# Kernel tuning notes

Hardware: AMD Instinct MI355X
Metric: run time of the kernel (lower is better)

Reference implementation:

```python
import jax, jax.numpy as jnp
import numpy as np

PATCH = 4      # patch_size
WIN = 8        # win_size (== win_stride, non-overlapping windows)
TAU = 0.05     # sinkhorn_tau
ITERS = 20     # sinkhorn_iters
EPS = 1e-6


def setup_inputs() -> dict:
    key = jax.random.key(0)
    k0, k1 = jax.random.split(key)
    B, C, H, W = 16, 4, 256, 256
    z0 = jax.random.normal(k0, (B, C, H, W), jnp.float32)
    z1 = jax.random.normal(k1, (B, C, H, W), jnp.float32)
    return {"z0": z0, "z1": z1}


def _token_feats(z):
    # patchify_latents + L2 normalize (F.normalize eps clamp). groupmean proj
    # is identity since d_match == token_dim.
    B, C, H, W = z.shape
    hp, wp = H // PATCH, W // PATCH
    t = z.reshape(B, C, hp, PATCH, wp, PATCH).transpose(0, 2, 4, 1, 3, 5)
    t = t.reshape(B, hp, wp, C * PATCH * PATCH)          # (B,hp,wp,D)
    n = jnp.maximum(jnp.sqrt(jnp.sum(t * t, axis=-1, keepdims=True)), EPS)
    return t / n


def _to_windows(f):
    B, hp, wp, D = f.shape
    nh, nw = hp // WIN, wp // WIN
    w = f.reshape(B, nh, WIN, nw, WIN, D).transpose(0, 1, 3, 2, 4, 5)
    return w.reshape(B * nh * nw, WIN * WIN, D)


def _sinkhorn_log(logits):
    # _sinkhorn_log_batch: alternate row (dim 2) / col (dim 1) logsumexp
    def step(lp, _):
        lp = lp - jax.nn.logsumexp(lp, axis=2, keepdims=True)
        lp = lp - jax.nn.logsumexp(lp, axis=1, keepdims=True)
        return lp, None
    lp, _ = jax.lax.scan(step, logits, None, length=ITERS)
    return lp


def _grid_sample_border(img, gx, gy):
    # F.grid_sample bilinear, padding_mode='border', align_corners=True,
    # with gx/gy already in absolute pixel coords (B,H,W).
    B, C, H, W = img.shape
    gx = jnp.clip(gx, 0.0, W - 1.0)
    gy = jnp.clip(gy, 0.0, H - 1.0)
    x0f = jnp.floor(gx); y0f = jnp.floor(gy)
    wx = (gx - x0f)[:, None]; wy = (gy - y0f)[:, None]   # (B,1,H,W)
    x0 = jnp.clip(x0f.astype(jnp.int32), 0, W - 1)
    x1 = jnp.clip(x0 + 1, 0, W - 1)
    y0 = jnp.clip(y0f.astype(jnp.int32), 0, H - 1)
    y1 = jnp.clip(y0 + 1, 0, H - 1)
    flat = img.reshape(B, C, H * W)

    def gat(yi, xi):
        idx = (yi * W + xi).reshape(B, 1, H * W)
        idx = jnp.broadcast_to(idx, (B, C, H * W))
        return jnp.take_along_axis(flat, idx, axis=2).reshape(B, C, H, W)

    v00 = gat(y0, x0); v01 = gat(y0, x1)
    v10 = gat(y1, x0); v11 = gat(y1, x1)
    return (v00 * (1 - wx) * (1 - wy) + v01 * wx * (1 - wy)
            + v10 * (1 - wx) * wy + v11 * wx * wy)


def reference(z0, z1):
    B, C, H, W = z0.shape
    hp, wp = H // PATCH, W // PATCH
    nh, nw = hp // WIN, wp // WIN
    f0 = _token_feats(z0)
    f1 = _token_feats(z1)
    w0 = _to_windows(f0)                                  # (BW, M, D)
    w1 = _to_windows(f1)
    logits = jnp.einsum('wid,wjd->wij', w0, w1) / TAU     # (BW, M, M)
    logp = _sinkhorn_log(logits)
    Pm = jax.nn.softmax(logp, axis=-1)                    # row-normalized plan
    # expected target position per source token (local window coords, x/y)
    ys, xs = jnp.meshgrid(jnp.arange(WIN), jnp.arange(WIN), indexing='ij')
    pos = jnp.stack([xs.ravel(), ys.ravel()], axis=-1).astype(z0.dtype)  # (M,2)
    disp = Pm @ pos - pos                                 # (BW, M, 2) token units
    disp = disp.reshape(B, nh, nw, WIN, WIN, 2).transpose(0, 1, 3, 2, 4, 5)
    disp = disp.reshape(B, hp, wp, 2)
    # token flow -> pixel flow (nearest upsample, scale by patch size)
    flow = jnp.repeat(jnp.repeat(disp, PATCH, axis=1), PATCH, axis=2) * PATCH
    yy, xx = jnp.meshgrid(jnp.arange(H, dtype=z0.dtype),
                          jnp.arange(W, dtype=z0.dtype), indexing='ij')
    gx = xx[None] + flow[..., 0]
    gy = yy[None] + flow[..., 1]
    return _grid_sample_border(z1, gx, gy)
```

## Files before the change

kernel.cpp:

```cpp
#include <hip/hip_runtime.h>
#include <math.h>


#define S0 68

__device__ __forceinline__ float rlane(float v, int l) {
    return __uint_as_float(__builtin_amdgcn_readlane(__float_as_uint(v), l));
}

__global__ __launch_bounds__(256, 1)
void skw_kernel(const float* __restrict__ z0, const float* __restrict__ z1,
                float* __restrict__ out) {
    __shared__ float f0 [64 * S0];
    __shared__ float f1t[64 * S0];
    __shared__ float Mw [4 * 64 * S0];
    __shared__ float psq0[256], psq1[256];
    __shared__ float invn0[64], invn1[64];
    __shared__ float dispxA[256], dispyA[256];

    const int t   = threadIdx.x;
    const int blk = blockIdx.x;
    const int b   = blk >> 4;
    const int wy  = (blk >> 1) & 7;
    const int wxq = blk & 1;
    const int Y0  = wy * 32;
    const int XB  = wxq * 128;

    const int xq = t & 7;
    const int yy = (t >> 3) & 31;
    const int mm = (yy >> 2) * 8 + xq;
    const int pi = yy & 3;

    const int wv   = t >> 6;
    const int lane = t & 63;

    #pragma unroll 1
    for (int w = 0; w < 4; ++w) {
        const int X0 = XB + w * 32;
        {
            const size_t base = (size_t)(b * 4) * 65536 + (size_t)(Y0 + yy) * 256 + X0 + xq * 4;
            const float* s0p = z0 + base;
            const float* s1p = z1 + base;
            float a0 = 0.f;
            #pragma unroll
            for (int c = 0; c < 4; ++c) {
                float4 vv = *(const float4*)(s0p + c * 65536);
                a0 += vv.x*vv.x + vv.y*vv.y + vv.z*vv.z + vv.w*vv.w;
                *(float4*)&f0[mm * S0 + c * 16 + pi * 4] = vv;
            }
            psq0[t] = a0;
            float a1 = 0.f;
            #pragma unroll
            for (int c = 0; c < 4; ++c) {
                float4 vv = *(const float4*)(s1p + c * 65536);
                a1 += vv.x*vv.x + vv.y*vv.y + vv.z*vv.z + vv.w*vv.w;
                const int d = c * 16 + pi * 4;
                f1t[(d+0)*S0 + mm] = vv.x;
                f1t[(d+1)*S0 + mm] = vv.y;
                f1t[(d+2)*S0 + mm] = vv.z;
                f1t[(d+3)*S0 + mm] = vv.w;
            }
            psq1[t] = a1;
        }
        __syncthreads();
        if (t < 128) {
            const int u2 = t & 63;
            const float* ps = (t < 64) ? psq0 : psq1;
            const int ti = u2 >> 3, tj = u2 & 7;
            float s = ps[(ti*4+0)*8+tj] + ps[(ti*4+1)*8+tj]
                    + ps[(ti*4+2)*8+tj] + ps[(ti*4+3)*8+tj];
            float r = 1.0f / fmaxf(sqrtf(s), 1e-6f);
            if (t < 64) invn0[u2] = r; else invn1[u2] = r;
        }
        __syncthreads();

        const int bi = t >> 4, bj = t & 15;
        float acc[4][4];
        #pragma unroll
        for (int r = 0; r < 4; ++r)
            #pragma unroll
            for (int s2 = 0; s2 < 4; ++s2) acc[r][s2] = 0.f;

        #pragma unroll 4
        for (int dc = 0; dc < 16; ++dc) {
            float4 A[4], Bv[4];
            #pragma unroll
            for (int r = 0; r < 4; ++r) A[r] = *(const float4*)&f0[(bi*4+r)*S0 + dc*4];
            #pragma unroll
            for (int dd = 0; dd < 4; ++dd) Bv[dd] = *(const float4*)&f1t[(dc*4+dd)*S0 + bj*4];
            #pragma unroll
            for (int r = 0; r < 4; ++r) {
                acc[r][0] += A[r].x*Bv[0].x + A[r].y*Bv[1].x + A[r].z*Bv[2].x + A[r].w*Bv[3].x;
                acc[r][1] += A[r].x*Bv[0].y + A[r].y*Bv[1].y + A[r].z*Bv[2].y + A[r].w*Bv[3].y;
                acc[r][2] += A[r].x*Bv[0].z + A[r].y*Bv[1].z + A[r].z*Bv[2].z + A[r].w*Bv[3].z;
                acc[r][3] += A[r].x*Bv[0].w + A[r].y*Bv[1].w + A[r].z*Bv[2].w + A[r].w*Bv[3].w;
            }
        }
        float si[4], sj[4];
        #pragma unroll
        for (int r = 0; r < 4; ++r)  si[r] = invn0[bi*4+r] * 20.0f;
        #pragma unroll
        for (int s2 = 0; s2 < 4; ++s2) sj[s2] = invn1[bj*4+s2];
        float* Mo = &Mw[w * (64 * S0)];
        #pragma unroll
        for (int r = 0; r < 4; ++r) {
            float4 o;
            o.x = acc[r][0]*si[r]*sj[0];
            o.y = acc[r][1]*si[r]*sj[1];
            o.z = acc[r][2]*si[r]*sj[2];
            o.w = acc[r][3]*si[r]*sj[3];
            *(float4*)&Mo[(bi*4+r)*S0 + bj*4] = o;
        }
        __syncthreads();
    }

    const float* Mb = &Mw[wv * (64 * S0)];
    float K[64], KT[64];
    #pragma unroll
    for (int j4 = 0; j4 < 16; ++j4) {
        float4 r4 = *(const float4*)&Mb[lane * S0 + j4 * 4];
        K[4*j4+0] = __expf(r4.x); K[4*j4+1] = __expf(r4.y);
        K[4*j4+2] = __expf(r4.z); K[4*j4+3] = __expf(r4.w);
    }
    #pragma unroll
    for (int j = 0; j < 64; ++j) KT[j] = __expf(Mb[j * S0 + lane]);

    float u, v;
    {
        float s0=0.f, s1=0.f, s2=0.f, s3=0.f;
        #pragma unroll
        for (int j = 0; j < 64; j += 4) {
            s0 += K[j]; s1 += K[j+1]; s2 += K[j+2]; s3 += K[j+3];
        }
        u = 1.0f / ((s0+s1) + (s2+s3));
    }
    #pragma unroll 1
    for (int it = 0; it < 19; ++it) {
        float s0=0.f, s1=0.f, s2=0.f, s3=0.f;
        #pragma unroll
        for (int j = 0; j < 64; j += 4) {
            s0 = fmaf(KT[j  ], rlane(u, j  ), s0);
            s1 = fmaf(KT[j+1], rlane(u, j+1), s1);
            s2 = fmaf(KT[j+2], rlane(u, j+2), s2);
            s3 = fmaf(KT[j+3], rlane(u, j+3), s3);
        }
        v = 1.0f / ((s0+s1) + (s2+s3));
        s0=0.f; s1=0.f; s2=0.f; s3=0.f;
        #pragma unroll
        for (int j = 0; j < 64; j += 4) {
            s0 = fmaf(K[j  ], rlane(v, j  ), s0);
            s1 = fmaf(K[j+1], rlane(v, j+1), s1);
            s2 = fmaf(K[j+2], rlane(v, j+2), s2);
            s3 = fmaf(K[j+3], rlane(v, j+3), s3);
        }
        u = 1.0f / ((s0+s1) + (s2+s3));
    }
    {
        float s0=0.f, s1=0.f, s2=0.f, s3=0.f;
        #pragma unroll
        for (int j = 0; j < 64; j += 4) {
            s0 = fmaf(KT[j  ], rlane(u, j  ), s0);
            s1 = fmaf(KT[j+1], rlane(u, j+1), s1);
            s2 = fmaf(KT[j+2], rlane(u, j+2), s2);
            s3 = fmaf(KT[j+3], rlane(u, j+3), s3);
        }
        v = 1.0f / ((s0+s1) + (s2+s3));
    }
    {
        float ss=0.f, sx=0.f, sy=0.f;
        #pragma unroll
        for (int j = 0; j < 64; ++j) {
            float pj = K[j] * rlane(v, j);
            ss += pj;
            sx = fmaf(pj, (float)(j & 7),  sx);
            sy = fmaf(pj, (float)(j >> 3), sy);
        }
        const float inv = 1.0f / ss;
        dispxA[t] = sx * inv - (float)(lane & 7);
        dispyA[t] = sy * inv - (float)(lane >> 3);
    }
    __syncthreads();

    #pragma unroll 2
    for (int rep = 0; rep < 16; ++rep) {
        const int p = rep * 256 + t;
        const int y = p >> 7;
        const int x = p & 127;
        const int m2 = ((y >> 2) << 3) + ((x & 31) >> 2);
        const int widx = (x >> 5) * 64 + m2;
        float gx = (float)(XB + x) + 4.0f * dispxA[widx];
        float gy = (float)(Y0 + y) + 4.0f * dispyA[widx];
        gx = fminf(fmaxf(gx, 0.0f), 255.0f);
        gy = fminf(fmaxf(gy, 0.0f), 255.0f);
        const float x0f = floorf(gx), y0f = floorf(gy);
        const float wxf = gx - x0f, wyf = gy - y0f;
        const int xi0 = (int)x0f, yi0 = (int)y0f;
        const int xi1 = min(xi0 + 1, 255), yi1 = min(yi0 + 1, 255);
        const float w00 = (1.f-wxf)*(1.f-wyf), w01 = wxf*(1.f-wyf);
        const float w10 = (1.f-wxf)*wyf,       w11 = wxf*wyf;
        const float* basep = z1 + (size_t)(b * 4) * 65536;
        #pragma unroll
        for (int c = 0; c < 4; ++c) {
            const float* pc = basep + c * 65536;
            const float v00 = pc[yi0*256 + xi0], v01 = pc[yi0*256 + xi1];
            const float v10 = pc[yi1*256 + xi0], v11 = pc[yi1*256 + xi1];
            out[((size_t)(b*4+c)*256 + (Y0+y))*256 + XB + x]
                = v00*w00 + v01*w01 + v10*w10 + v11*w11;
        }
    }
}

extern "C" void kernel_launch(void* const* d_in, const int* in_sizes, int n_in,
                              void* d_out, int out_size, void* d_ws, size_t ws_size,
                              hipStream_t stream) {
    (void)in_sizes; (void)n_in; (void)d_ws; (void)ws_size; (void)out_size;
    const float* z0 = (const float*)d_in[0];
    const float* z1 = (const float*)d_in[1];
    float* out = (float*)d_out;
    skw_kernel<<<dim3(256), dim3(256), 0, stream>>>(z0, z1, out);
}
```

Measured before the change: 108.0 us.

## Split work to one window per block with 1024 blocks and smaller LDS

Each block now handles a single 8x8 token window instead of four, so the grid grows from 256 to 1024 blocks and LDS use drops because the four-window score buffer is gone and the score matrix reuses the f0 buffer. The f1 tile is stored row-major instead of transposed, and launch bounds now allow three blocks per CU for better occupancy and latency hiding. Only one wavefront per block runs the serial Sinkhorn iterations while the other three sit idle, and the wave chosen rotates with the block index so the work spreads across SIMDs. This trades per-block wave utilisation during Sinkhorn for more parallel blocks across the device's CUs.

```diff
diff --git a/kernel.cpp b/kernel.cpp
--- a/kernel.cpp
+++ b/kernel.cpp
@@ -8,188 +8,170 @@
     return __uint_as_float(__builtin_amdgcn_readlane(__float_as_uint(v), l));
 }
 
-__global__ __launch_bounds__(256, 1)
+__global__ __launch_bounds__(256, 3)
 void skw_kernel(const float* __restrict__ z0, const float* __restrict__ z1,
                 float* __restrict__ out) {
-    __shared__ float f0 [64 * S0];
-    __shared__ float f1t[64 * S0];
-    __shared__ float Mw [4 * 64 * S0];
+    __shared__ float f0[64 * S0];
+    __shared__ float f1[64 * S0];
     __shared__ float psq0[256], psq1[256];
     __shared__ float invn0[64], invn1[64];
-    __shared__ float dispxA[256], dispyA[256];
+    __shared__ float dispx[64], dispy[64];
 
     const int t   = threadIdx.x;
     const int blk = blockIdx.x;
-    const int b   = blk >> 4;
-    const int wy  = (blk >> 1) & 7;
-    const int wxq = blk & 1;
-    const int Y0  = wy * 32;
-    const int XB  = wxq * 128;
+    const int b   = blk >> 6;
+    const int wy  = (blk >> 3) & 7;
+    const int wx  = blk & 7;
+    const int Y0  = wy * 32, X0 = wx * 32;
 
     const int xq = t & 7;
     const int yy = (t >> 3) & 31;
     const int mm = (yy >> 2) * 8 + xq;
     const int pi = yy & 3;
 
-    const int wv   = t >> 6;
+    {
+        const size_t base = (size_t)(b * 4) * 65536 + (size_t)(Y0 + yy) * 256 + X0 + xq * 4;
+        const float* s0p = z0 + base;
+        const float* s1p = z1 + base;
+        float a0 = 0.f, a1 = 0.f;
+        #pragma unroll
+        for (int c = 0; c < 4; ++c) {
+            float4 v0 = *(const float4*)(s0p + c * 65536);
+            float4 v1 = *(const float4*)(s1p + c * 65536);
+            a0 += v0.x*v0.x + v0.y*v0.y + v0.z*v0.z + v0.w*v0.w;
+            a1 += v1.x*v1.x + v1.y*v1.y + v1.z*v1.z + v1.w*v1.w;
+            *(float4*)&f0[mm * S0 + c * 16 + pi * 4] = v0;
+            *(float4*)&f1[mm * S0 + c * 16 + pi * 4] = v1;
+        }
+        psq0[t] = a0; psq1[t] = a1;
+    }
+    __syncthreads();
+    if (t < 128) {
+        const int u2 = t & 63;
+        const float* ps = (t < 64) ? psq0 : psq1;
+        const int ti = u2 >> 3, tj = u2 & 7;
+        float s = ps[(ti*4+0)*8+tj] + ps[(ti*4+1)*8+tj]
+                + ps[(ti*4+2)*8+tj] + ps[(ti*4+3)*8+tj];
+        float r = 1.0f / fmaxf(sqrtf(s), 1e-6f);
+        if (t < 64) invn0[u2] = r; else invn1[u2] = r;
+    }
+    __syncthreads();
+
+    const int bi = t >> 4, bj = t & 15;
+    float acc[4][4];
+    #pragma unroll
+    for (int r = 0; r < 4; ++r)
+        #pragma unroll
+        for (int s2 = 0; s2 < 4; ++s2) acc[r][s2] = 0.f;
+
+    #pragma unroll 4
+    for (int dc = 0; dc < 16; ++dc) {
+        float4 A[4], Bv[4];
+        #pragma unroll
+        for (int r = 0; r < 4; ++r)  A[r]  = *(const float4*)&f0[(bi*4+r)*S0 + dc*4];
+        #pragma unroll
+        for (int s2 = 0; s2 < 4; ++s2) Bv[s2] = *(const float4*)&f1[(bj*4+s2)*S0 + dc*4];
+        #pragma unroll
+        for (int r = 0; r < 4; ++r)
+            #pragma unroll
+            for (int s2 = 0; s2 < 4; ++s2)
+                acc[r][s2] += A[r].x*Bv[s2].x + A[r].y*Bv[s2].y
+                            + A[r].z*Bv[s2].z + A[r].w*Bv[s2].w;
+    }
+    float si[4], sj[4];
+    #pragma unroll
+    for (int r = 0; r < 4; ++r)  si[r] = invn0[bi*4+r] * 20.0f;
+    #pragma unroll
+    for (int s2 = 0; s2 < 4; ++s2) sj[s2] = invn1[bj*4+s2];
+    __syncthreads();
+    float* Mm = f0;
+    #pragma unroll
+    for (int r = 0; r < 4; ++r) {
+        float4 o;
+        o.x = acc[r][0]*si[r]*sj[0];
+        o.y = acc[r][1]*si[r]*sj[1];
+        o.z = acc[r][2]*si[r]*sj[2];
+        o.w = acc[r][3]*si[r]*sj[3];
+        *(float4*)&Mm[(bi*4+r)*S0 + bj*4] = o;
+    }
+    __syncthreads();
+
     const int lane = t & 63;
-
-    #pragma unroll 1
-    for (int w = 0; w < 4; ++w) {
-        const int X0 = XB + w * 32;
+    if ((t >> 6) == (blk & 3)) {
+        float K[64], KT[64];
+        #pragma unroll
+        for (int j4 = 0; j4 < 16; ++j4) {
+            float4 r4 = *(const float4*)&Mm[lane * S0 + j4 * 4];
+            K[4*j4+0] = __expf(r4.x); K[4*j4+1] = __expf(r4.y);
+            K[4*j4+2] = __expf(r4.z); K[4*j4+3] = __expf(r4.w);
+        }
+        #pragma unroll
+        for (int j = 0; j < 64; ++j) KT[j] = __expf(Mm[j * S0 + lane]);
+
+        float u, v;
         {
-            const size_t base = (size_t)(b * 4) * 65536 + (size_t)(Y0 + yy) * 256 + X0 + xq * 4;
-            const float* s0p = z0 + base;
-            const float* s1p = z1 + base;
-            float a0 = 0.f;
-            #pragma unroll
-            for (int c = 0; c < 4; ++c) {
-                float4 vv = *(const float4*)(s0p + c * 65536);
-                a0 += vv.x*vv.x + vv.y*vv.y + vv.z*vv.z + vv.w*vv.w;
-                *(float4*)&f0[mm * S0 + c * 16 + pi * 4] = vv;
-            }
-            psq0[t] = a0;
-            float a1 = 0.f;
-            #pragma unroll
-            for (int c = 0; c < 4; ++c) {
-                float4 vv = *(const float4*)(s1p + c * 65536);
-                a1 += vv.x*vv.x + vv.y*vv.y + vv.z*vv.z + vv.w*vv.w;
-                const int d = c * 16 + pi * 4;
-                f1t[(d+0)*S0 + mm] = vv.x;
-                f1t[(d+1)*S0 + mm] = vv.y;
-                f1t[(d+2)*S0 + mm] = vv.z;
-                f1t[(d+3)*S0 + mm] = vv.w;
-            }
-            psq1[t] = a1;
-        }
-        __syncthreads();
-        if (t < 128) {
-            const int u2 = t & 63;
-            const float* ps = (t < 64) ? psq0 : psq1;
-            const int ti = u2 >> 3, tj = u2 & 7;
-            float s = ps[(ti*4+0)*8+tj] + ps[(ti*4+1)*8+tj]
-                    + ps[(ti*4+2)*8+tj] + ps[(ti*4+3)*8+tj];
-            float r = 1.0f / fmaxf(sqrtf(s), 1e-6f);
-            if (t < 64) invn0[u2] = r; else invn1[u2] = r;
-        }
-        __syncthreads();
-
-        const int bi = t >> 4, bj = t & 15;
-        float acc[4][4];
-        #pragma unroll
-        for (int r = 0; r < 4; ++r)
-            #pragma unroll
-            for (int s2 = 0; s2 < 4; ++s2) acc[r][s2] = 0.f;
-
-        #pragma unroll 4
-        for (int dc = 0; dc < 16; ++dc) {
-            float4 A[4], Bv[4];
-            #pragma unroll
-            for (int r = 0; r < 4; ++r) A[r] = *(const float4*)&f0[(bi*4+r)*S0 + dc*4];
-            #pragma unroll
-            for (int dd = 0; dd < 4; ++dd) Bv[dd] = *(const float4*)&f1t[(dc*4+dd)*S0 + bj*4];
-            #pragma unroll
-            for (int r = 0; r < 4; ++r) {
-                acc[r][0] += A[r].x*Bv[0].x + A[r].y*Bv[1].x + A[r].z*Bv[2].x + A[r].w*Bv[3].x;
-                acc[r][1] += A[r].x*Bv[0].y + A[r].y*Bv[1].y + A[r].z*Bv[2].y + A[r].w*Bv[3].y;
-                acc[r][2] += A[r].x*Bv[0].z + A[r].y*Bv[1].z + A[r].z*Bv[2].z + A[r].w*Bv[3].z;
-                acc[r][3] += A[r].x*Bv[0].w + A[r].y*Bv[1].w + A[r].z*Bv[2].w + A[r].w*Bv[3].w;
-            }
-        }
-        float si[4], sj[4];
-        #pragma unroll
-        for (int r = 0; r < 4; ++r)  si[r] = invn0[bi*4+r] * 20.0f;
-        #pragma unroll
-        for (int s2 = 0; s2 < 4; ++s2) sj[s2] = invn1[bj*4+s2];
-        float* Mo = &Mw[w * (64 * S0)];
-        #pragma unroll
-        for (int r = 0; r < 4; ++r) {
-            float4 o;
-            o.x = acc[r][0]*si[r]*sj[0];
-            o.y = acc[r][1]*si[r]*sj[1];
-            o.z = acc[r][2]*si[r]*sj[2];
-            o.w = acc[r][3]*si[r]*sj[3];
-            *(float4*)&Mo[(bi*4+r)*S0 + bj*4] = o;
-        }
-        __syncthreads();
-    }
-
-    const float* Mb = &Mw[wv * (64 * S0)];
-    float K[64], KT[64];
-    #pragma unroll
-    for (int j4 = 0; j4 < 16; ++j4) {
-        float4 r4 = *(const float4*)&Mb[lane * S0 + j4 * 4];
-        K[4*j4+0] = __expf(r4.x); K[4*j4+1] = __expf(r4.y);
-        K[4*j4+2] = __expf(r4.z); K[4*j4+3] = __expf(r4.w);
-    }
-    #pragma unroll
-    for (int j = 0; j < 64; ++j) KT[j] = __expf(Mb[j * S0 + lane]);
-
-    float u, v;
-    {
-        float s0=0.f, s1=0.f, s2=0.f, s3=0.f;
-        #pragma unroll
-        for (int j = 0; j < 64; j += 4) {
-            s0 += K[j]; s1 += K[j+1]; s2 += K[j+2]; s3 += K[j+3];
-        }
-        u = 1.0f / ((s0+s1) + (s2+s3));
-    }
-    #pragma unroll 1
-    for (int it = 0; it < 19; ++it) {
-        float s0=0.f, s1=0.f, s2=0.f, s3=0.f;
-        #pragma unroll
-        for (int j = 0; j < 64; j += 4) {
-            s0 = fmaf(KT[j  ], rlane(u, j  ), s0);
-            s1 = fmaf(KT[j+1], rlane(u, j+1), s1);
-            s2 = fmaf(KT[j+2], rlane(u, j+2), s2);
-            s3 = fmaf(KT[j+3], rlane(u, j+3), s3);
-        }
-        v = 1.0f / ((s0+s1) + (s2+s3));
-        s0=0.f; s1=0.f; s2=0.f; s3=0.f;
-        #pragma unroll
-        for (int j = 0; j < 64; j += 4) {
-            s0 = fmaf(K[j  ], rlane(v, j  ), s0);
-            s1 = fmaf(K[j+1], rlane(v, j+1), s1);
-            s2 = fmaf(K[j+2], rlane(v, j+2), s2);
-            s3 = fmaf(K[j+3], rlane(v, j+3), s3);
-        }
-        u = 1.0f / ((s0+s1) + (s2+s3));
-    }
-    {
-        float s0=0.f, s1=0.f, s2=0.f, s3=0.f;
-        #pragma unroll
-        for (int j = 0; j < 64; j += 4) {
-            s0 = fmaf(KT[j  ], rlane(u, j  ), s0);
-            s1 = fmaf(KT[j+1], rlane(u, j+1), s1);
-            s2 = fmaf(KT[j+2], rlane(u, j+2), s2);
-            s3 = fmaf(KT[j+3], rlane(u, j+3), s3);
-        }
-        v = 1.0f / ((s0+s1) + (s2+s3));
-    }
-    {
-        float ss=0.f, sx=0.f, sy=0.f;
-        #pragma unroll
-        for (int j = 0; j < 64; ++j) {
-            float pj = K[j] * rlane(v, j);
-            ss += pj;
-            sx = fmaf(pj, (float)(j & 7),  sx);
-            sy = fmaf(pj, (float)(j >> 3), sy);
-        }
-        const float inv = 1.0f / ss;
-        dispxA[t] = sx * inv - (float)(lane & 7);
-        dispyA[t] = sy * inv - (float)(lane >> 3);
-    }
-    __syncthreads();
-
-    #pragma unroll 2
-    for (int rep = 0; rep < 16; ++rep) {
+            float s0=0.f, s1=0.f, s2=0.f, s3=0.f;
+            #pragma unroll
+            for (int j = 0; j < 64; j += 4) {
+                s0 += K[j]; s1 += K[j+1]; s2 += K[j+2]; s3 += K[j+3];
+            }
+            u = 1.0f / ((s0+s1) + (s2+s3));
+        }
+        #pragma unroll 1
+        for (int it = 0; it < 19; ++it) {
+            float s0=0.f, s1=0.f, s2=0.f, s3=0.f;
+            #pragma unroll
+            for (int j = 0; j < 64; j += 4) {
+                s0 = fmaf(KT[j  ], rlane(u, j  ), s0);
+                s1 = fmaf(KT[j+1], rlane(u, j+1), s1);
+                s2 = fmaf(KT[j+2], rlane(u, j+2), s2);
+                s3 = fmaf(KT[j+3], rlane(u, j+3), s3);
+            }
+            v = 1.0f / ((s0+s1) + (s2+s3));
+            s0=0.f; s1=0.f; s2=0.f; s3=0.f;
+            #pragma unroll
+            for (int j = 0; j < 64; j += 4) {
+                s0 = fmaf(K[j  ], rlane(v, j  ), s0);
+                s1 = fmaf(K[j+1], rlane(v, j+1), s1);
+                s2 = fmaf(K[j+2], rlane(v, j+2), s2);
+                s3 = fmaf(K[j+3], rlane(v, j+3), s3);
+            }
+            u = 1.0f / ((s0+s1) + (s2+s3));
+        }
+        {
+            float s0=0.f, s1=0.f, s2=0.f, s3=0.f;
+            #pragma unroll
+            for (int j = 0; j < 64; j += 4) {
+                s0 = fmaf(KT[j  ], rlane(u, j  ), s0);
+                s1 = fmaf(KT[j+1], rlane(u, j+1), s1);
+                s2 = fmaf(KT[j+2], rlane(u, j+2), s2);
+                s3 = fmaf(KT[j+3], rlane(u, j+3), s3);
+            }
+            v = 1.0f / ((s0+s1) + (s2+s3));
+        }
+        {
+            float ss=0.f, sx=0.f, sy=0.f;
+            #pragma unroll
+            for (int j = 0; j < 64; ++j) {
+                float pj = K[j] * rlane(v, j);
+                ss += pj;
+                sx = fmaf(pj, (float)(j & 7),  sx);
+                sy = fmaf(pj, (float)(j >> 3), sy);
+            }
+            const float inv = 1.0f / ss;
+            dispx[lane] = sx * inv - (float)(lane & 7);
+            dispy[lane] = sy * inv - (float)(lane >> 3);
+        }
+    }
+    __syncthreads();
+
+    #pragma unroll
+    for (int rep = 0; rep < 4; ++rep) {
         const int p = rep * 256 + t;
-        const int y = p >> 7;
-        const int x = p & 127;
-        const int m2 = ((y >> 2) << 3) + ((x & 31) >> 2);
-        const int widx = (x >> 5) * 64 + m2;
-        float gx = (float)(XB + x) + 4.0f * dispxA[widx];
-        float gy = (float)(Y0 + y) + 4.0f * dispyA[widx];
+        const int y = p >> 5, x = p & 31;
+        const int m2 = (y >> 2) * 8 + (x >> 2);
+        float gx = (float)(X0 + x) + 4.0f * dispx[m2];
+        float gy = (float)(Y0 + y) + 4.0f * dispy[m2];
         gx = fminf(fmaxf(gx, 0.0f), 255.0f);
         gy = fminf(fmaxf(gy, 0.0f), 255.0f);
         const float x0f = floorf(gx), y0f = floorf(gy);
@@ -204,7 +186,7 @@
             const float* pc = basep + c * 65536;
             const float v00 = pc[yi0*256 + xi0], v01 = pc[yi0*256 + xi1];
             const float v10 = pc[yi1*256 + xi0], v11 = pc[yi1*256 + xi1];
-            out[((size_t)(b*4+c)*256 + (Y0+y))*256 + XB + x]
+            out[((size_t)(b*4+c)*256 + (Y0+y))*256 + X0 + x]
                 = v00*w00 + v01*w01 + v10*w10 + v11*w11;
         }
     }
@@ -217,5 +199,5 @@
     const float* z0 = (const float*)d_in[0];
     const float* z1 = (const float*)d_in[1];
     float* out = (float*)d_out;
-    skw_kernel<<<dim3(256), dim3(256), 0, stream>>>(z0, z1, out);
+    skw_kernel<<<dim3(1024), dim3(256), 0, stream>>>(z0, z1, out);
 }
```

Measured after the change: 119.0 us. +10.2%, slower.
